# Optimization experiments

Hardware: AMD Instinct MI355X
Metric: run time of the kernel (lower is better)

## Reference

```python
import jax, jax.numpy as jnp
import numpy as np

GAMMA = 0.015625  # 1/D


def setup_inputs() -> dict:
    key = jax.random.key(0)
    k1, k2 = jax.random.split(key)
    data = jax.random.normal(k1, (8192, 64), dtype=jnp.float32)
    support_vectors = jax.random.normal(k2, (8192, 64), dtype=jnp.float32)
    return {"data": data, "support_vectors": support_vectors}


def reference(data, support_vectors):
    # RBF kernel matrix: K[i,j] = exp(-gamma * ||data_i - sv_j||^2)
    # instead of the original per-row Python loop.
    x_sq = jnp.sum(data * data, axis=1, keepdims=True)          # [N, 1]
    y_sq = jnp.sum(support_vectors * support_vectors, axis=1)   # [M]
    cross = data @ support_vectors.T                             # [N, M]
    d2 = jnp.maximum(x_sq + y_sq[None, :] - 2.0 * cross, 0.0)
    return jnp.exp(-GAMMA * d2)
```

## Files before the change

kernel.cpp:

```cpp
#include <hip/hip_runtime.h>
#include <hip/hip_bf16.h>
#include <string.h>

#define GAMMA 0.015625f
#define D 64
#define CT 4

typedef short bf16x8 __attribute__((ext_vector_type(8)));
typedef float floatx16 __attribute__((ext_vector_type(16)));

__device__ __forceinline__ bf16x8 cvt8(const float* __restrict__ p, float& ss) {
    const float4 a = *(const float4*)p;
    const float4 b = *(const float4*)(p + 4);
    const float f[8] = {a.x, a.y, a.z, a.w, b.x, b.y, b.z, b.w};
    bf16x8 r;
#pragma unroll
    for (int i = 0; i < 8; ++i) {
        __hip_bfloat16 h = __float2bfloat16(f[i]);
        short s;
        memcpy(&s, &h, sizeof(short));
        r[i] = s;
        const float bv = __bfloat162float(h);
        ss = fmaf(bv, bv, ss);
    }
    return r;
}

__global__ __launch_bounds__(256) void rbf_fused32(const float* __restrict__ A,
                                                   const float* __restrict__ B,
                                                   float* __restrict__ out,
                                                   int M) {
    const int wid  = threadIdx.x >> 6;
    const int lane = threadIdx.x & 63;
    const int r32  = lane & 31;
    const int h    = lane >> 5;

    const long row0 = (long)blockIdx.y * 128 + (wid >> 1) * 64;
    const long colW = (long)blockIdx.x * (128 * CT) + (wid & 1) * 64;

    bf16x8 af[2][4];
    float xnorm[2];
#pragma unroll
    for (int mb = 0; mb < 2; ++mb) {
        const float* p = A + (row0 + mb * 32 + r32) * D + h * 8;
        float s = 0.f;
#pragma unroll
        for (int ks = 0; ks < 4; ++ks)
            af[mb][ks] = cvt8(p + ks * 16, s);
        s += __shfl_xor(s, 32, 64);
        xnorm[mb] = s;
    }

    for (int ct = 0; ct < CT; ++ct) {
        const long colT = colW + (long)ct * 128;

        bf16x8 bfr[2][4];
        float ynorm[2];
#pragma unroll
        for (int nb = 0; nb < 2; ++nb) {
            const float* p = B + (colT + nb * 32 + r32) * D + h * 8;
            float s = 0.f;
#pragma unroll
            for (int ks = 0; ks < 4; ++ks)
                bfr[nb][ks] = cvt8(p + ks * 16, s);
            s += __shfl_xor(s, 32, 64);
            ynorm[nb] = s;
        }

        floatx16 acc[2][2] = {};
#pragma unroll
        for (int ks = 0; ks < 4; ++ks)
#pragma unroll
            for (int mb = 0; mb < 2; ++mb)
#pragma unroll
                for (int nb = 0; nb < 2; ++nb)
                    acc[mb][nb] = __builtin_amdgcn_mfma_f32_32x32x16_bf16(
                        af[mb][ks], bfr[nb][ks], acc[mb][nb], 0, 0, 0);

#pragma unroll
        for (int mb = 0; mb < 2; ++mb) {
            float xnv[16];
#pragma unroll
            for (int rg = 0; rg < 16; ++rg)
                xnv[rg] = __shfl(xnorm[mb], (rg & 3) + 8 * (rg >> 2) + 4 * h, 64);
#pragma unroll
            for (int nb = 0; nb < 2; ++nb) {
                const long col = colT + nb * 32 + r32;
                const float yn = ynorm[nb];
                float* op = out + (row0 + mb * 32) * (long)M + col;
#pragma unroll
                for (int rg = 0; rg < 16; ++rg) {
                    const int rl = (rg & 3) + 8 * (rg >> 2) + 4 * h;
                    float d2 = fmaxf(xnv[rg] + yn - 2.0f * acc[mb][nb][rg], 0.0f);
                    op[(long)rl * M] = __expf(-GAMMA * d2);
                }
            }
        }
    }
}

__global__ __launch_bounds__(256) void rbf_naive(const float* __restrict__ X,
                                                 const float* __restrict__ Y,
                                                 float* __restrict__ out,
                                                 int N, int M) {
    long idx = (long)blockIdx.x * blockDim.x + threadIdx.x;
    if (idx >= (long)N * M) return;
    long i = idx / M, j = idx % M;
    float s = 0.0f;
#pragma unroll
    for (int k = 0; k < D; ++k) {
        float d = X[i * D + k] - Y[j * D + k];
        s = fmaf(d, d, s);
    }
    out[idx] = __expf(-GAMMA * s);
}

extern "C" void kernel_launch(void* const* d_in, const int* in_sizes, int n_in,
                              void* d_out, int out_size, void* d_ws, size_t ws_size,
                              hipStream_t stream) {
    const float* data = (const float*)d_in[0];
    const float* sv   = (const float*)d_in[1];
    float* out = (float*)d_out;
    const int N = in_sizes[0] / D;
    const int M = in_sizes[1] / D;

    if ((N % 128) == 0 && (M % (128 * CT)) == 0) {
        dim3 grid(M / (128 * CT), N / 128);
        hipLaunchKernelGGL(rbf_fused32, grid, dim3(256), 0, stream,
                           data, sv, out, M);
    } else {
        long total = (long)N * M;
        long blocks = (total + 255) / 256;
        hipLaunchKernelGGL(rbf_naive, dim3((unsigned)blocks), dim3(256), 0, stream,
                           data, sv, out, N, M);
    }
}
```

Measured before the change: 300.3 us.

## Precompute bf16 operands and norms in a prep kernel, use nontemporal output stores

Adds a prep kernel that converts both inputs to bf16 once and computes their squared norms into workspace. The main GEMM kernel then loads bf16 fragments and precomputed norms directly, so B is no longer re-converted by every row block. Output stores become nontemporal, and CT drops from 4 to 2, which doubles the grid size. The cost is an extra kernel launch and a workspace round trip, plus a fallback to the naive kernel if the workspace is too small.

Result: faster. 272.7 us (-9.2%).

```diff
diff --git a/kernel.cpp b/kernel.cpp
--- a/kernel.cpp
+++ b/kernel.cpp
@@ -4,7 +4,7 @@
 
 #define GAMMA 0.015625f
 #define D 64
-#define CT 4
+#define CT 2
 
 typedef short bf16x8 __attribute__((ext_vector_type(8)));
 typedef float floatx16 __attribute__((ext_vector_type(16)));
@@ -26,10 +26,38 @@
     return r;
 }
 
-__global__ __launch_bounds__(256) void rbf_fused32(const float* __restrict__ A,
-                                                   const float* __restrict__ B,
-                                                   float* __restrict__ out,
-                                                   int M) {
+__global__ __launch_bounds__(256) void prep_all(const float* __restrict__ srcA,
+                                                const float* __restrict__ srcB,
+                                                short* __restrict__ dstA,
+                                                short* __restrict__ dstB,
+                                                float* __restrict__ nrmA,
+                                                float* __restrict__ nrmB,
+                                                int nA, int nTot) {
+    const int idx = blockIdx.x * 256 + threadIdx.x;
+    const int row = idx >> 3;
+    const int sub = idx & 7;
+    if (row >= nTot) return;
+    const float* src;
+    short* dst;
+    float* nrm;
+    int r;
+    if (row < nA) { src = srcA; dst = dstA; nrm = nrmA; r = row; }
+    else          { src = srcB; dst = dstB; nrm = nrmB; r = row - nA; }
+    float ss = 0.f;
+    const bf16x8 v = cvt8(src + (size_t)r * D + sub * 8, ss);
+    *(bf16x8*)(dst + (size_t)r * D + sub * 8) = v;
+    ss += __shfl_xor(ss, 1, 64);
+    ss += __shfl_xor(ss, 2, 64);
+    ss += __shfl_xor(ss, 4, 64);
+    if (sub == 0) nrm[r] = ss;
+}
+
+__global__ __launch_bounds__(256) void rbf_gemm32(const short* __restrict__ A,
+                                                  const short* __restrict__ B,
+                                                  const float* __restrict__ xsq,
+                                                  const float* __restrict__ ysq,
+                                                  float* __restrict__ out,
+                                                  int M) {
     const int wid  = threadIdx.x >> 6;
     const int lane = threadIdx.x & 63;
     const int r32  = lane & 31;
@@ -39,32 +67,28 @@
     const long colW = (long)blockIdx.x * (128 * CT) + (wid & 1) * 64;
 
     bf16x8 af[2][4];
-    float xnorm[2];
+    float xn_l[2];
 #pragma unroll
     for (int mb = 0; mb < 2; ++mb) {
-        const float* p = A + (row0 + mb * 32 + r32) * D + h * 8;
-        float s = 0.f;
+        const short* p = A + (row0 + mb * 32 + r32) * D + h * 8;
 #pragma unroll
         for (int ks = 0; ks < 4; ++ks)
-            af[mb][ks] = cvt8(p + ks * 16, s);
-        s += __shfl_xor(s, 32, 64);
-        xnorm[mb] = s;
+            af[mb][ks] = *(const bf16x8*)(p + ks * 16);
+        xn_l[mb] = xsq[row0 + mb * 32 + r32];
     }
 
     for (int ct = 0; ct < CT; ++ct) {
         const long colT = colW + (long)ct * 128;
 
         bf16x8 bfr[2][4];
-        float ynorm[2];
+        float yn_l[2];
 #pragma unroll
         for (int nb = 0; nb < 2; ++nb) {
-            const float* p = B + (colT + nb * 32 + r32) * D + h * 8;
-            float s = 0.f;
+            const short* p = B + (colT + nb * 32 + r32) * D + h * 8;
 #pragma unroll
             for (int ks = 0; ks < 4; ++ks)
-                bfr[nb][ks] = cvt8(p + ks * 16, s);
-            s += __shfl_xor(s, 32, 64);
-            ynorm[nb] = s;
+                bfr[nb][ks] = *(const bf16x8*)(p + ks * 16);
+            yn_l[nb] = ysq[colT + nb * 32 + r32];
         }
 
         floatx16 acc[2][2] = {};
@@ -82,17 +106,16 @@
             float xnv[16];
 #pragma unroll
             for (int rg = 0; rg < 16; ++rg)
-                xnv[rg] = __shfl(xnorm[mb], (rg & 3) + 8 * (rg >> 2) + 4 * h, 64);
+                xnv[rg] = __shfl(xn_l[mb], (rg & 3) + 8 * (rg >> 2) + 4 * h, 64);
 #pragma unroll
             for (int nb = 0; nb < 2; ++nb) {
-                const long col = colT + nb * 32 + r32;
-                const float yn = ynorm[nb];
-                float* op = out + (row0 + mb * 32) * (long)M + col;
+                const float yn = yn_l[nb];
+                float* op = out + (row0 + mb * 32) * (long)M + colT + nb * 32 + r32;
 #pragma unroll
                 for (int rg = 0; rg < 16; ++rg) {
                     const int rl = (rg & 3) + 8 * (rg >> 2) + 4 * h;
-                    float d2 = fmaxf(xnv[rg] + yn - 2.0f * acc[mb][nb][rg], 0.0f);
-                    op[(long)rl * M] = __expf(-GAMMA * d2);
+                    const float d2 = fmaxf(xnv[rg] + yn - 2.0f * acc[mb][nb][rg], 0.0f);
+                    __builtin_nontemporal_store(__expf(-GAMMA * d2), op + (long)rl * M);
                 }
             }
         }
@@ -124,10 +147,24 @@
     const int N = in_sizes[0] / D;
     const int M = in_sizes[1] / D;
 
-    if ((N % 128) == 0 && (M % (128 * CT)) == 0) {
+    const size_t bfA  = (size_t)N * D * sizeof(short);
+    const size_t bfB  = (size_t)M * D * sizeof(short);
+    const size_t need = bfA + bfB + (size_t)(N + M) * sizeof(float);
+
+    if (ws_size >= need && (N % 128) == 0 && (M % (128 * CT)) == 0) {
+        char* ws = (char*)d_ws;
+        short* Abf = (short*)ws;
+        short* Bbf = (short*)(ws + bfA);
+        float* xsq = (float*)(ws + bfA + bfB);
+        float* ysq = xsq + N;
+
+        const int nTot = N + M;
+        const int prep_blocks = (nTot * 8 + 255) / 256;
+        hipLaunchKernelGGL(prep_all, dim3(prep_blocks), dim3(256), 0, stream,
+                           data, sv, Abf, Bbf, xsq, ysq, N, nTot);
         dim3 grid(M / (128 * CT), N / 128);
-        hipLaunchKernelGGL(rbf_fused32, grid, dim3(256), 0, stream,
-                           data, sv, out, M);
+        hipLaunchKernelGGL(rbf_gemm32, grid, dim3(256), 0, stream,
+                           Abf, Bbf, xsq, ysq, out, M);
     } else {
         long total = (long)N * M;
         long blocks = (total + 255) / 256;
```
